# Kernel tuning notes

Measured on AMD Instinct MI355X. Metric: run time of the kernel, lower is better.

## Reference

```python
import jax, jax.numpy as jnp
import numpy as np

N = 100000        # nodes
E_RAND = 1600000  # random edges (avg degree 16)
D_IN = 64
D_OUT = 64


def setup_inputs() -> dict:
    key = jax.random.key(0)
    k1, k2, k3, k4, k5 = jax.random.split(key, 5)
    x = jax.random.normal(k1, (N, D_IN), dtype=jnp.float32)
    rows = jax.random.randint(k2, (E_RAND,), 0, N)
    cols = jax.random.randint(k3, (E_RAND,), 0, N)
    loops = jnp.arange(N)  # self loops appended at the end (matches remove+add_self_loops order)
    edge_index = jnp.stack([jnp.concatenate([rows, loops]),
                            jnp.concatenate([cols, loops])]).astype(jnp.int64)
    W = (jax.random.normal(k4, (D_IN, D_OUT), dtype=jnp.float32) / np.float32(np.sqrt(D_IN)))
    b = jax.random.normal(k5, (D_OUT,), dtype=jnp.float32) * 0.01
    return {"x": x, "edge_index": edge_index, "W": W, "b": b}


def reference(x, edge_index, W, b):
    row, col = edge_index[0], edge_index[1]
    # lin(x[row]) == (x @ W + b)[row]; transform once then gather (cheaper, same math)
    xl = x @ W + b                      # [N, D_OUT]
    x_i = xl[row]                       # [E, D_OUT] gather by destination
    x_j = xl[col]                       # [E, D_OUT] gather by source
    alpha = jnp.sum(x_i * x_j, axis=-1)  # [E] per-edge score
    alpha = jax.nn.leaky_relu(alpha, negative_slope=0.2)
    # segment-wise softmax over neighborhoods keyed by row
    m = jax.ops.segment_max(alpha, row, num_segments=N)
    m = jnp.where(jnp.isfinite(m), m, 0.0)   # isolated nodes -> -inf max, neutralize
    e = jnp.exp(alpha - m[row])
    s = jax.ops.segment_sum(e, row, num_segments=N)
    alpha = e / (s[row] + 1e-16)
    # dropout(p=0.6) skipped: reference runs in eval mode (deterministic)
    out = jax.ops.segment_sum(x_j * alpha[:, None], row, num_segments=N)  # [N, D_OUT]
    return out
```

## Files before the change

kernel.cpp:

```cpp
#include <hip/hip_runtime.h>
#include <hip/hip_bf16.h>


#define LEAKY_SLOPE 0.2f
#define BK_SHIFT 6
#define BK_NODES 64
#define CAP 1408
#define NBMAX 1600
#define CH 8192
#define NCH_MAX 256

typedef __attribute__((ext_vector_type(8))) short short8;
typedef __attribute__((ext_vector_type(4))) float f32x4;

struct HiLo { short hi, lo; };

__device__ __forceinline__ HiLo split2(float f) {
    HiLo r;
    unsigned u = __float_as_uint(f);
    r.hi = (short)(u >> 16);
    float fh = __uint_as_float(u & 0xFFFF0000u);
    r.lo = (short)(__float_as_uint(f - fh) >> 16);
    return r;
}

union PreShMem {
    struct { short wt_hi[64 * 72]; short wt_lo[64 * 72]; } lin;
    struct { int cnt[NBMAX], scn[NBMAX], pos[NBMAX], segsum[1024]; } ms;
};

__global__ __launch_bounds__(1024) void k_pre(const float* __restrict__ x,
                                              const float* __restrict__ W,
                                              const float* __restrict__ b,
                                              const int* __restrict__ row,
                                              const int* __restrict__ col,
                                              float* __restrict__ xl,
                                              unsigned short* __restrict__ xlh,
                                              int* __restrict__ ofs,
                                              unsigned* __restrict__ staging,
                                              int N, int E, int NB,
                                              int ntiles, int nch) {
    __shared__ PreShMem sh;
    int tid = threadIdx.x;

    if ((int)blockIdx.x < nch) {
        int vbk = (int)blockIdx.x;
        int e0 = vbk * CH;
        int e1 = min(E, e0 + CH);

        for (int i = tid; i < NB; i += 1024) { sh.ms.cnt[i] = 0; sh.ms.pos[i] = 0; }
        __syncthreads();

        for (int e = e0 + tid; e < e1; e += 1024)
            atomicAdd(&sh.ms.cnt[row[e] >> BK_SHIFT], 1);
        __syncthreads();

        int segbeg = tid * 2;
        int segend = min(NB, segbeg + 2);
        int s = 0;
        for (int i = segbeg; i < segend; ++i) { int v = sh.ms.cnt[i]; sh.ms.scn[i] = s; s += v; }
        sh.ms.segsum[tid] = s;
        __syncthreads();
        for (int o = 1; o < 1024; o <<= 1) {
            int v = (tid >= o) ? sh.ms.segsum[tid - o] : 0;
            __syncthreads();
            sh.ms.segsum[tid] += v;
            __syncthreads();
        }
        int segoff = (tid == 0) ? 0 : sh.ms.segsum[tid - 1];
        for (int i = segbeg; i < segend; ++i) sh.ms.scn[i] += segoff;
        __syncthreads();

        int* orow = ofs + (size_t)vbk * (NB + 1);
        for (int i = tid; i < NB; i += 1024) orow[i] = sh.ms.scn[i];
        if (tid == 0) orow[NB] = e1 - e0;

        unsigned* stg = staging + (size_t)vbk * CH;
        for (int e = e0 + tid; e < e1; e += 1024) {
            int r = row[e], c = col[e];
            int bkt = r >> BK_SHIFT;
            int p = sh.ms.scn[bkt] + atomicAdd(&sh.ms.pos[bkt], 1);
            stg[p] = ((unsigned)(r & (BK_NODES - 1)) << 17) | (unsigned)c;
        }
    } else {
        for (int i = tid; i < 4096; i += 1024) {
            int k = i >> 6, n = i & 63;
            HiLo h = split2(W[i]);
            sh.lin.wt_hi[n * 72 + k] = h.hi;
            sh.lin.wt_lo[n * 72 + k] = h.lo;
        }
        __syncthreads();

        int wave = tid >> 6, lane = tid & 63;
        int tile = ((int)blockIdx.x - nch) * 16 + wave;
        if (tile >= ntiles) return;
        int node0 = tile * 16;
        int m = lane & 15;
        int quad = lane >> 4;

        f32x4 acc[4] = {{0.f, 0.f, 0.f, 0.f}, {0.f, 0.f, 0.f, 0.f},
                        {0.f, 0.f, 0.f, 0.f}, {0.f, 0.f, 0.f, 0.f}};

#pragma unroll
        for (int ks = 0; ks < 64; ks += 32) {
            const float* xr = x + (size_t)(node0 + m) * 64 + ks + quad * 8;
            float4 xa = *(const float4*)xr;
            float4 xb = *(const float4*)(xr + 4);
            short8 a_hi, a_lo;
            {
                HiLo h0 = split2(xa.x), h1 = split2(xa.y), h2 = split2(xa.z), h3 = split2(xa.w);
                HiLo h4 = split2(xb.x), h5 = split2(xb.y), h6 = split2(xb.z), h7 = split2(xb.w);
                a_hi[0] = h0.hi; a_lo[0] = h0.lo;  a_hi[1] = h1.hi; a_lo[1] = h1.lo;
                a_hi[2] = h2.hi; a_lo[2] = h2.lo;  a_hi[3] = h3.hi; a_lo[3] = h3.lo;
                a_hi[4] = h4.hi; a_lo[4] = h4.lo;  a_hi[5] = h5.hi; a_lo[5] = h5.lo;
                a_hi[6] = h6.hi; a_lo[6] = h6.lo;  a_hi[7] = h7.hi; a_lo[7] = h7.lo;
            }
#pragma unroll
            for (int g = 0; g < 4; ++g) {
                int n = g * 16 + m;
                int off = n * 72 + ks + quad * 8;
                short8 bh = *(const short8*)&sh.lin.wt_hi[off];
                short8 bl = *(const short8*)&sh.lin.wt_lo[off];
                acc[g] = __builtin_amdgcn_mfma_f32_16x16x32_bf16(a_hi, bh, acc[g], 0, 0, 0);
                acc[g] = __builtin_amdgcn_mfma_f32_16x16x32_bf16(a_lo, bh, acc[g], 0, 0, 0);
                acc[g] = __builtin_amdgcn_mfma_f32_16x16x32_bf16(a_hi, bl, acc[g], 0, 0, 0);
            }
        }

#pragma unroll
        for (int g = 0; g < 4; ++g) {
            float bias = b[g * 16 + m];
#pragma unroll
            for (int r = 0; r < 4; ++r) {
                int node = node0 + quad * 4 + r;
                if (node < N) {
                    float v = acc[g][r] + bias;
                    xl[(size_t)node * 64 + g * 16 + m] = v;
                    xlh[(size_t)node * 64 + g * 16 + m] =
                        (unsigned short)(__float_as_uint(v) >> 16);
                }
            }
        }
    }
}

__device__ __forceinline__ float red8(float d) {
    d += __shfl_xor(d, 1, 64);
    d += __shfl_xor(d, 2, 64);
    d += __shfl_xor(d, 4, 64);
    return d;
}

__device__ __forceinline__ void bf8_to_f8(uint4 u, float4& a, float4& b) {
    a.x = __uint_as_float(u.x << 16);
    a.y = __uint_as_float(u.x & 0xFFFF0000u);
    a.z = __uint_as_float(u.y << 16);
    a.w = __uint_as_float(u.y & 0xFFFF0000u);
    b.x = __uint_as_float(u.z << 16);
    b.y = __uint_as_float(u.z & 0xFFFF0000u);
    b.z = __uint_as_float(u.w << 16);
    b.w = __uint_as_float(u.w & 0xFFFF0000u);
}

__device__ __forceinline__ float dot4(float4 a, float4 b) {
    return a.x * b.x + a.y * b.y + a.z * b.z + a.w * b.w;
}

__device__ __forceinline__ void upd8(float& m, float& l, float4& A, float4& B,
                                     float a, float4 xa, float4 xb) {
    if (a <= m) {
        float p = __expf(a - m);
        l += p;
        A.x += p * xa.x; A.y += p * xa.y; A.z += p * xa.z; A.w += p * xa.w;
        B.x += p * xb.x; B.y += p * xb.y; B.z += p * xb.z; B.w += p * xb.w;
    } else {
        float sc = __expf(m - a);
        l = l * sc + 1.0f;
        A.x = A.x * sc + xa.x; A.y = A.y * sc + xa.y;
        A.z = A.z * sc + xa.z; A.w = A.w * sc + xa.w;
        B.x = B.x * sc + xb.x; B.y = B.y * sc + xb.y;
        B.z = B.z * sc + xb.z; B.w = B.w * sc + xb.w;
        m = a;
    }
}

__global__ __launch_bounds__(256) void k_sortfused(const float* __restrict__ xl,
                                                   const unsigned short* __restrict__ xlh,
                                                   const unsigned* __restrict__ staging,
                                                   const int* __restrict__ ofs,
                                                   float* __restrict__ out,
                                                   int N, int NB, int nch) {
    __shared__ int raw[CAP];
    __shared__ int colsh[CAP];
    __shared__ int deg[BK_NODES], sc[BK_NODES], cur[BK_NODES];
    __shared__ int lenarr[NCH_MAX];
    __shared__ int chbeg[NCH_MAX + 1];
    __shared__ int chofs[NCH_MAX];

    int bkt = blockIdx.x;
    int tid = threadIdx.x;

    if (tid < NCH_MAX) {
        int len = 0;
        if (tid < nch) {
            const int* orow = ofs + (size_t)tid * (NB + 1);
            int o0 = orow[bkt], o1 = orow[bkt + 1];
            chofs[tid] = o0;
            len = o1 - o0;
        }
        lenarr[tid] = len;
    }
    __syncthreads();
    for (int o = 1; o < NCH_MAX; o <<= 1) {
        int v = 0;
        if (tid < NCH_MAX && tid >= o) v = lenarr[tid - o];
        __syncthreads();
        if (tid < NCH_MAX) lenarr[tid] += v;
        __syncthreads();
    }
    if (tid <= nch) chbeg[tid] = (tid == 0) ? 0 : lenarr[tid - 1];
    __syncthreads();

    int cnt = min(chbeg[nch], CAP);

    for (int i = tid; i < cnt; i += 256) {
        int lo = 0, hi = nch - 1;
        while (lo < hi) {
            int mid = (lo + hi + 1) >> 1;
            if (chbeg[mid] <= i) lo = mid; else hi = mid - 1;
        }
        raw[i] = (int)staging[(size_t)lo * CH + chofs[lo] + (i - chbeg[lo])];
    }

    if (tid < BK_NODES) { deg[tid] = 0; cur[tid] = 0; }
    __syncthreads();

    for (int e = tid; e < cnt; e += 256) atomicAdd(&deg[((unsigned)raw[e]) >> 17], 1);
    __syncthreads();

    if (tid < BK_NODES) sc[tid] = deg[tid];
    __syncthreads();
#pragma unroll
    for (int o = 1; o < BK_NODES; o <<= 1) {
        int v = 0;
        if (tid < BK_NODES && tid >= o) v = sc[tid - o];
        __syncthreads();
        if (tid < BK_NODES) sc[tid] += v;
        __syncthreads();
    }

    for (int e = tid; e < cnt; e += 256) {
        unsigned pk = (unsigned)raw[e];
        int rl = pk >> 17;
        int p = sc[rl] - deg[rl] + atomicAdd(&cur[rl], 1);
        colsh[p] = (int)(pk & 0x1FFFFu);
    }
    __syncthreads();

    int grp = tid >> 3;
    int g = tid & 7;
    const uint4* xh4 = (const uint4*)xlh;
    for (int n0 = grp; n0 < BK_NODES; n0 += 32) {
        int node = bkt * BK_NODES + n0;
        if (node >= N) continue;
        int beg = sc[n0] - deg[n0];
        int end = sc[n0];
        float4 xia = ((const float4*)xl)[(size_t)node * 16 + 2 * g];
        float4 xib = ((const float4*)xl)[(size_t)node * 16 + 2 * g + 1];

        float m = -INFINITY, l = 0.0f;
        float4 accA = {0.f, 0.f, 0.f, 0.f};
        float4 accB = {0.f, 0.f, 0.f, 0.f};

        int e = beg;
        for (; e + 4 <= end; e += 4) {
            int c0 = colsh[e], c1 = colsh[e + 1], c2 = colsh[e + 2], c3 = colsh[e + 3];
            uint4 u0 = xh4[(size_t)c0 * 8 + g];
            uint4 u1 = xh4[(size_t)c1 * 8 + g];
            uint4 u2 = xh4[(size_t)c2 * 8 + g];
            uint4 u3 = xh4[(size_t)c3 * 8 + g];
            float4 xa0, xb0, xa1, xb1, xa2, xb2, xa3, xb3;
            bf8_to_f8(u0, xa0, xb0);
            bf8_to_f8(u1, xa1, xb1);
            bf8_to_f8(u2, xa2, xb2);
            bf8_to_f8(u3, xa3, xb3);
            float d0 = red8(dot4(xia, xa0) + dot4(xib, xb0));
            float d1 = red8(dot4(xia, xa1) + dot4(xib, xb1));
            float d2 = red8(dot4(xia, xa2) + dot4(xib, xb2));
            float d3 = red8(dot4(xia, xa3) + dot4(xib, xb3));
            upd8(m, l, accA, accB, (d0 >= 0.f) ? d0 : LEAKY_SLOPE * d0, xa0, xb0);
            upd8(m, l, accA, accB, (d1 >= 0.f) ? d1 : LEAKY_SLOPE * d1, xa1, xb1);
            upd8(m, l, accA, accB, (d2 >= 0.f) ? d2 : LEAKY_SLOPE * d2, xa2, xb2);
            upd8(m, l, accA, accB, (d3 >= 0.f) ? d3 : LEAKY_SLOPE * d3, xa3, xb3);
        }
        for (; e < end; ++e) {
            int c = colsh[e];
            uint4 u = xh4[(size_t)c * 8 + g];
            float4 xa, xb;
            bf8_to_f8(u, xa, xb);
            float d = red8(dot4(xia, xa) + dot4(xib, xb));
            upd8(m, l, accA, accB, (d >= 0.f) ? d : LEAKY_SLOPE * d, xa, xb);
        }
        float inv = 1.0f / (l + 1e-16f);
        float4 oA = {accA.x * inv, accA.y * inv, accA.z * inv, accA.w * inv};
        float4 oB = {accB.x * inv, accB.y * inv, accB.z * inv, accB.w * inv};
        ((float4*)out)[(size_t)node * 16 + 2 * g] = oA;
        ((float4*)out)[(size_t)node * 16 + 2 * g + 1] = oB;
    }
}

extern "C" void kernel_launch(void* const* d_in, const int* in_sizes, int n_in,
                              void* d_out, int out_size, void* d_ws, size_t ws_size,
                              hipStream_t stream) {
    const float* x = (const float*)d_in[0];
    const int* ei = (const int*)d_in[1];
    const float* W = (const float*)d_in[2];
    const float* b = (const float*)d_in[3];

    const int N = in_sizes[0] / 64;
    const int E = in_sizes[1] / 2;
    const int NO = N * 64;
    const int NB = (N + BK_NODES - 1) >> BK_SHIFT;
    const int NCH = (E + CH - 1) / CH;
    const int* row = ei;
    const int* col = ei + E;

    float* out = (float*)d_out;

    float* ws = (float*)d_ws;
    float* xl           = ws;
    unsigned short* xlh = (unsigned short*)(xl + (size_t)NO);
    int* ofs            = (int*)(xlh + (size_t)NO);
    unsigned* staging   = (unsigned*)(ofs + (size_t)NCH * (NB + 1));

    const int ntiles = (N + 15) / 16;
    const int lblocks = (ntiles + 15) / 16;

    k_pre<<<NCH + lblocks, 1024, 0, stream>>>(x, W, b, row, col, xl, xlh,
                                              ofs, staging, N, E, NB, ntiles, NCH);
    k_sortfused<<<NB, 256, 0, stream>>>(xl, xlh, staging, ofs, out, N, NB, NCH);
}
```

Baseline: 161.4 us.

## Replace chunked counting-sort partition with global atomic cursor bins

```diff
diff --git a/kernel.cpp b/kernel.cpp
--- a/kernel.cpp
+++ b/kernel.cpp
@@ -6,9 +6,8 @@
 #define BK_SHIFT 6
 #define BK_NODES 64
 #define CAP 1408
-#define NBMAX 1600
-#define CH 8192
-#define NCH_MAX 256
+#define CAPG 288
+#define MS_BLOCKS 512
 
 typedef __attribute__((ext_vector_type(8))) short short8;
 typedef __attribute__((ext_vector_type(4))) float f32x4;
@@ -24,75 +23,62 @@
     return r;
 }
 
-union PreShMem {
-    struct { short wt_hi[64 * 72]; short wt_lo[64 * 72]; } lin;
-    struct { int cnt[NBMAX], scn[NBMAX], pos[NBMAX], segsum[1024]; } ms;
-};
-
-__global__ __launch_bounds__(1024) void k_pre(const float* __restrict__ x,
-                                              const float* __restrict__ W,
-                                              const float* __restrict__ b,
-                                              const int* __restrict__ row,
-                                              const int* __restrict__ col,
-                                              float* __restrict__ xl,
-                                              unsigned short* __restrict__ xlh,
-                                              int* __restrict__ ofs,
-                                              unsigned* __restrict__ staging,
-                                              int N, int E, int NB,
-                                              int ntiles, int nch) {
-    __shared__ PreShMem sh;
+__global__ __launch_bounds__(256) void k_pre(const float* __restrict__ x,
+                                             const float* __restrict__ W,
+                                             const float* __restrict__ b,
+                                             const int* __restrict__ row,
+                                             const int* __restrict__ col,
+                                             float* __restrict__ xl,
+                                             unsigned short* __restrict__ xlh,
+                                             int* __restrict__ cursor,
+                                             unsigned* __restrict__ staging,
+                                             int N, int E, int ntiles) {
+    __shared__ __align__(16) short Wt_hi[64 * 72];
+    __shared__ __align__(16) short Wt_lo[64 * 72];
     int tid = threadIdx.x;
 
-    if ((int)blockIdx.x < nch) {
-        int vbk = (int)blockIdx.x;
-        int e0 = vbk * CH;
-        int e1 = min(E, e0 + CH);
-
-        for (int i = tid; i < NB; i += 1024) { sh.ms.cnt[i] = 0; sh.ms.pos[i] = 0; }
-        __syncthreads();
-
-        for (int e = e0 + tid; e < e1; e += 1024)
-            atomicAdd(&sh.ms.cnt[row[e] >> BK_SHIFT], 1);
-        __syncthreads();
-
-        int segbeg = tid * 2;
-        int segend = min(NB, segbeg + 2);
-        int s = 0;
-        for (int i = segbeg; i < segend; ++i) { int v = sh.ms.cnt[i]; sh.ms.scn[i] = s; s += v; }
-        sh.ms.segsum[tid] = s;
-        __syncthreads();
-        for (int o = 1; o < 1024; o <<= 1) {
-            int v = (tid >= o) ? sh.ms.segsum[tid - o] : 0;
-            __syncthreads();
-            sh.ms.segsum[tid] += v;
-            __syncthreads();
-        }
-        int segoff = (tid == 0) ? 0 : sh.ms.segsum[tid - 1];
-        for (int i = segbeg; i < segend; ++i) sh.ms.scn[i] += segoff;
-        __syncthreads();
-
-        int* orow = ofs + (size_t)vbk * (NB + 1);
-        for (int i = tid; i < NB; i += 1024) orow[i] = sh.ms.scn[i];
-        if (tid == 0) orow[NB] = e1 - e0;
-
-        unsigned* stg = staging + (size_t)vbk * CH;
-        for (int e = e0 + tid; e < e1; e += 1024) {
+    if ((int)blockIdx.x < MS_BLOCKS) {
+        const int ech = (E + MS_BLOCKS - 1) / MS_BLOCKS;
+        int e0 = blockIdx.x * ech;
+        int e1 = min(E, e0 + ech);
+        int x8 = (int)blockIdx.x & 7;
+
+        int e = e0 + tid;
+        for (; e + 3 * 256 < e1; e += 4 * 256) {
+            int r0 = row[e], c0 = col[e];
+            int r1 = row[e + 256], c1 = col[e + 256];
+            int r2 = row[e + 512], c2 = col[e + 512];
+            int r3 = row[e + 768], c3 = col[e + 768];
+            int cell0 = (r0 >> BK_SHIFT) * 8 + x8;
+            int cell1 = (r1 >> BK_SHIFT) * 8 + x8;
+            int cell2 = (r2 >> BK_SHIFT) * 8 + x8;
+            int cell3 = (r3 >> BK_SHIFT) * 8 + x8;
+            int p0 = atomicAdd(&cursor[cell0 * 16], 1);
+            int p1 = atomicAdd(&cursor[cell1 * 16], 1);
+            int p2 = atomicAdd(&cursor[cell2 * 16], 1);
+            int p3 = atomicAdd(&cursor[cell3 * 16], 1);
+            if (p0 < CAPG) staging[(size_t)cell0 * CAPG + p0] = ((unsigned)(r0 & 63) << 17) | (unsigned)c0;
+            if (p1 < CAPG) staging[(size_t)cell1 * CAPG + p1] = ((unsigned)(r1 & 63) << 17) | (unsigned)c1;
+            if (p2 < CAPG) staging[(size_t)cell2 * CAPG + p2] = ((unsigned)(r2 & 63) << 17) | (unsigned)c2;
+            if (p3 < CAPG) staging[(size_t)cell3 * CAPG + p3] = ((unsigned)(r3 & 63) << 17) | (unsigned)c3;
+        }
+        for (; e < e1; e += 256) {
             int r = row[e], c = col[e];
-            int bkt = r >> BK_SHIFT;
-            int p = sh.ms.scn[bkt] + atomicAdd(&sh.ms.pos[bkt], 1);
-            stg[p] = ((unsigned)(r & (BK_NODES - 1)) << 17) | (unsigned)c;
+            int cell = (r >> BK_SHIFT) * 8 + x8;
+            int p = atomicAdd(&cursor[cell * 16], 1);
+            if (p < CAPG) staging[(size_t)cell * CAPG + p] = ((unsigned)(r & 63) << 17) | (unsigned)c;
         }
     } else {
-        for (int i = tid; i < 4096; i += 1024) {
+        for (int i = tid; i < 4096; i += 256) {
             int k = i >> 6, n = i & 63;
             HiLo h = split2(W[i]);
-            sh.lin.wt_hi[n * 72 + k] = h.hi;
-            sh.lin.wt_lo[n * 72 + k] = h.lo;
+            Wt_hi[n * 72 + k] = h.hi;
+            Wt_lo[n * 72 + k] = h.lo;
         }
         __syncthreads();
 
         int wave = tid >> 6, lane = tid & 63;
-        int tile = ((int)blockIdx.x - nch) * 16 + wave;
+        int tile = ((int)blockIdx.x - MS_BLOCKS) * 4 + wave;
         if (tile >= ntiles) return;
         int node0 = tile * 16;
         int m = lane & 15;
@@ -119,8 +105,8 @@
             for (int g = 0; g < 4; ++g) {
                 int n = g * 16 + m;
                 int off = n * 72 + ks + quad * 8;
-                short8 bh = *(const short8*)&sh.lin.wt_hi[off];
-                short8 bl = *(const short8*)&sh.lin.wt_lo[off];
+                short8 bh = *(const short8*)&Wt_hi[off];
+                short8 bl = *(const short8*)&Wt_lo[off];
                 acc[g] = __builtin_amdgcn_mfma_f32_16x16x32_bf16(a_hi, bh, acc[g], 0, 0, 0);
                 acc[g] = __builtin_amdgcn_mfma_f32_16x16x32_bf16(a_lo, bh, acc[g], 0, 0, 0);
                 acc[g] = __builtin_amdgcn_mfma_f32_16x16x32_bf16(a_hi, bl, acc[g], 0, 0, 0);
@@ -187,55 +173,40 @@
 __global__ __launch_bounds__(256) void k_sortfused(const float* __restrict__ xl,
                                                    const unsigned short* __restrict__ xlh,
                                                    const unsigned* __restrict__ staging,
-                                                   const int* __restrict__ ofs,
-                                                   float* __restrict__ out,
-                                                   int N, int NB, int nch) {
-    __shared__ int raw[CAP];
+                                                   const int* __restrict__ cursor,
+                                                   float* __restrict__ out, int N) {
     __shared__ int colsh[CAP];
     __shared__ int deg[BK_NODES], sc[BK_NODES], cur[BK_NODES];
-    __shared__ int lenarr[NCH_MAX];
-    __shared__ int chbeg[NCH_MAX + 1];
-    __shared__ int chofs[NCH_MAX];
+    __shared__ int beg[9];
+    __shared__ int clen[8];
 
     int bkt = blockIdx.x;
     int tid = threadIdx.x;
 
-    if (tid < NCH_MAX) {
-        int len = 0;
-        if (tid < nch) {
-            const int* orow = ofs + (size_t)tid * (NB + 1);
-            int o0 = orow[bkt], o1 = orow[bkt + 1];
-            chofs[tid] = o0;
-            len = o1 - o0;
-        }
-        lenarr[tid] = len;
-    }
-    __syncthreads();
-    for (int o = 1; o < NCH_MAX; o <<= 1) {
-        int v = 0;
-        if (tid < NCH_MAX && tid >= o) v = lenarr[tid - o];
-        __syncthreads();
-        if (tid < NCH_MAX) lenarr[tid] += v;
-        __syncthreads();
-    }
-    if (tid <= nch) chbeg[tid] = (tid == 0) ? 0 : lenarr[tid - 1];
-    __syncthreads();
-
-    int cnt = min(chbeg[nch], CAP);
+    if (tid < 8) {
+        int cn = cursor[(bkt * 8 + tid) * 16];
+        clen[tid] = min(cn, CAPG);
+    }
+    if (tid < BK_NODES) { deg[tid] = 0; cur[tid] = 0; }
+    __syncthreads();
+    if (tid == 0) {
+        int s = 0;
+#pragma unroll
+        for (int i = 0; i < 8; ++i) { beg[i] = s; s += clen[i]; }
+        beg[8] = s;
+    }
+    __syncthreads();
+
+    int cnt = min(beg[8], CAP);
+    const unsigned* stg0 = staging + (size_t)bkt * 8 * CAPG;
 
     for (int i = tid; i < cnt; i += 256) {
-        int lo = 0, hi = nch - 1;
-        while (lo < hi) {
-            int mid = (lo + hi + 1) >> 1;
-            if (chbeg[mid] <= i) lo = mid; else hi = mid - 1;
-        }
-        raw[i] = (int)staging[(size_t)lo * CH + chofs[lo] + (i - chbeg[lo])];
-    }
-
-    if (tid < BK_NODES) { deg[tid] = 0; cur[tid] = 0; }
-    __syncthreads();
-
-    for (int e = tid; e < cnt; e += 256) atomicAdd(&deg[((unsigned)raw[e]) >> 17], 1);
+        int x = 0;
+#pragma unroll
+        for (int k = 1; k < 8; ++k) if (i >= beg[k]) x = k;
+        unsigned pk = stg0[(size_t)x * CAPG + (i - beg[x])];
+        atomicAdd(&deg[pk >> 17], 1);
+    }
     __syncthreads();
 
     if (tid < BK_NODES) sc[tid] = deg[tid];
@@ -249,8 +220,11 @@
         __syncthreads();
     }
 
-    for (int e = tid; e < cnt; e += 256) {
-        unsigned pk = (unsigned)raw[e];
+    for (int i = tid; i < cnt; i += 256) {
+        int x = 0;
+#pragma unroll
+        for (int k = 1; k < 8; ++k) if (i >= beg[k]) x = k;
+        unsigned pk = stg0[(size_t)x * CAPG + (i - beg[x])];
         int rl = pk >> 17;
         int p = sc[rl] - deg[rl] + atomicAdd(&cur[rl], 1);
         colsh[p] = (int)(pk & 0x1FFFFu);
@@ -263,8 +237,8 @@
     for (int n0 = grp; n0 < BK_NODES; n0 += 32) {
         int node = bkt * BK_NODES + n0;
         if (node >= N) continue;
-        int beg = sc[n0] - deg[n0];
-        int end = sc[n0];
+        int beg_e = sc[n0] - deg[n0];
+        int end_e = sc[n0];
         float4 xia = ((const float4*)xl)[(size_t)node * 16 + 2 * g];
         float4 xib = ((const float4*)xl)[(size_t)node * 16 + 2 * g + 1];
 
@@ -272,8 +246,8 @@
         float4 accA = {0.f, 0.f, 0.f, 0.f};
         float4 accB = {0.f, 0.f, 0.f, 0.f};
 
-        int e = beg;
-        for (; e + 4 <= end; e += 4) {
+        int e = beg_e;
+        for (; e + 4 <= end_e; e += 4) {
             int c0 = colsh[e], c1 = colsh[e + 1], c2 = colsh[e + 2], c3 = colsh[e + 3];
             uint4 u0 = xh4[(size_t)c0 * 8 + g];
             uint4 u1 = xh4[(size_t)c1 * 8 + g];
@@ -293,7 +267,7 @@
             upd8(m, l, accA, accB, (d2 >= 0.f) ? d2 : LEAKY_SLOPE * d2, xa2, xb2);
             upd8(m, l, accA, accB, (d3 >= 0.f) ? d3 : LEAKY_SLOPE * d3, xa3, xb3);
         }
-        for (; e < end; ++e) {
+        for (; e < end_e; ++e) {
             int c = colsh[e];
             uint4 u = xh4[(size_t)c * 8 + g];
             float4 xa, xb;
@@ -321,7 +295,6 @@
     const int E = in_sizes[1] / 2;
     const int NO = N * 64;
     const int NB = (N + BK_NODES - 1) >> BK_SHIFT;
-    const int NCH = (E + CH - 1) / CH;
     const int* row = ei;
     const int* col = ei + E;
 
@@ -330,13 +303,14 @@
     float* ws = (float*)d_ws;
     float* xl           = ws;
     unsigned short* xlh = (unsigned short*)(xl + (size_t)NO);
-    int* ofs            = (int*)(xlh + (size_t)NO);
-    unsigned* staging   = (unsigned*)(ofs + (size_t)NCH * (NB + 1));
+    int* cursor         = (int*)(xlh + (size_t)NO);
+    unsigned* staging   = (unsigned*)(cursor + (size_t)NB * 8 * 16);
 
     const int ntiles = (N + 15) / 16;
-    const int lblocks = (ntiles + 15) / 16;
-
-    k_pre<<<NCH + lblocks, 1024, 0, stream>>>(x, W, b, row, col, xl, xlh,
-                                              ofs, staging, N, E, NB, ntiles, NCH);
-    k_sortfused<<<NB, 256, 0, stream>>>(xl, xlh, staging, ofs, out, N, NB, NCH);
-}
+    const int lblocks = (ntiles + 3) / 4;
+
+    hipMemsetAsync(cursor, 0, (size_t)NB * 8 * 16 * sizeof(int), stream);
+    k_pre<<<MS_BLOCKS + lblocks, 256, 0, stream>>>(x, W, b, row, col, xl, xlh,
+                                                   cursor, staging, N, E, ntiles);
+    k_sortfused<<<NB, 256, 0, stream>>>(xl, xlh, staging, cursor, out, N);
+}
```

Measured after the change: 231.3 us. 1.43x slower.
